# Kernel optimization log

Hardware: AMD Instinct MI355X
Metric: run time of the kernel (lower is better)

## Reference

```python
import jax, jax.numpy as jnp
import numpy as np

N, E = 50000, 800000
F_IN, HID, CLS, K = 128, 128, 40, 4


def setup_inputs() -> dict:
    key = jax.random.key(0)
    ks = jax.random.split(key, 6)
    x = jax.random.normal(ks[0], (N, F_IN), jnp.float32)
    edge_src = jax.random.randint(ks[1], (E,), 0, N, jnp.int32)
    edge_dst = jax.random.randint(ks[2], (E,), 0, N, jnp.int32)
    glorot = lambda k, sh, fan: jax.random.normal(k, sh, jnp.float32) * np.float32(1.0 / np.sqrt(fan))
    W0 = glorot(ks[3], (K, F_IN, HID), F_IN)
    W1 = glorot(ks[4], (K, HID, HID), HID)
    W2 = glorot(ks[5], (K, HID, CLS), HID)
    b0 = jnp.zeros((HID,), jnp.float32)
    b1 = jnp.zeros((HID,), jnp.float32)
    b2 = jnp.zeros((CLS,), jnp.float32)
    return dict(x=x, edge_src=edge_src, edge_dst=edge_dst,
                W0=W0, b0=b0, W1=W1, b1=b1, W2=W2, b2=b2)


def _cheb_edge_norm(edge_src, edge_dst, n):
    # PyG ChebConv 'sym' norm with lambda_max=2: scaled Laplacian
    # L_hat = 2L/lambda_max - I = -D^{-1/2} A D^{-1/2}  (diagonal is exactly 0)
    ones = jnp.ones(edge_src.shape[0], jnp.float32)
    deg = jax.ops.segment_sum(ones, edge_src, num_segments=n)
    dinv = jnp.where(deg > 0, jax.lax.rsqrt(jnp.maximum(deg, 1.0)), 0.0)
    return -dinv[edge_src] * dinv[edge_dst]  # [E]


def _cheb_conv(x, edge_src, edge_dst, w_norm, W, b, n):
    # Chebyshev recurrence: Tx0 = x, Tx1 = L_hat x, Tx_k = 2 L_hat Tx_{k-1} - Tx_{k-2}
    def lhat(t):  # SpMM: out[dst] += w * t[src]
        return jax.ops.segment_sum(t[edge_src] * w_norm[:, None], edge_dst, num_segments=n)

    Tx0 = x
    out = Tx0 @ W[0]
    Tx1 = lhat(Tx0)
    out = out + Tx1 @ W[1]
    for k in range(2, W.shape[0]):
        Tx2 = 2.0 * lhat(Tx1) - Tx0
        out = out + Tx2 @ W[k]
        Tx0, Tx1 = Tx1, Tx2
    return out + b


def reference(x, edge_src, edge_dst, W0, b0, W1, b1, W2, b2):
    n = x.shape[0]
    w_norm = _cheb_edge_norm(edge_src, edge_dst, n)
    h = x
    x1 = h
    for W, b in ((W0, b0), (W1, b1), (W2, b2)):
        x1 = _cheb_conv(h, edge_src, edge_dst, w_norm, W, b, n)
        h = jax.nn.relu(x1)  # dropout(p=0.6) is identity in eval mode
    # original returns log_softmax of the LAST conv's pre-activation x1
    return jax.nn.log_softmax(x1, axis=1)
```

## Files before the change

### kernel.cpp

```cpp
#include <hip/hip_runtime.h>
#include <math.h>

#define NN 50000
#define NE 800000
#define FDIM 128
#define CLS 40
#define AW 512
#define ZW 256
#define RSLOT 64

typedef __attribute__((ext_vector_type(8))) short short8v;
typedef __attribute__((ext_vector_type(8))) unsigned short ushort8v;
typedef __attribute__((ext_vector_type(4))) float f32x4;

__device__ inline float b2f(unsigned short u) {
    union { unsigned int i; float f; } v; v.i = ((unsigned)u) << 16; return v.f;
}
__device__ inline unsigned short f2b(float f) {
    unsigned int x = __float_as_uint(f);
    unsigned int r = (x + 0x7fffu + ((x >> 16) & 1u)) >> 16;
    return (unsigned short)r;
}


__global__ void zero_k(int* degi, int* fill) {
    int i = blockIdx.x * blockDim.x + threadIdx.x;
    if (i < NN) { degi[i] = 0; fill[i] = 0; }
}

#define NB_ES   782
#define NB_CVT  3125
#define NB_WH   256
#define NB_WZ   128

__global__ __launch_bounds__(256) void prep_k(
        const int4* __restrict__ esrc4, const int4* __restrict__ edst4,
        int* degi, int* fill, int* __restrict__ ews,
        const float* __restrict__ x, unsigned short* __restrict__ Ab,
        const float* __restrict__ W0, const float* __restrict__ W1,
        const float* __restrict__ W2,
        unsigned short* __restrict__ Wt0, unsigned short* __restrict__ Wt1,
        unsigned short* __restrict__ Wz) {
    int b = blockIdx.x;
    int tid = threadIdx.x;
    if (b < NB_ES) {
        int e = b * 256 + tid;
        if (e < NE / 4) {
            int4 s = esrc4[e], d = edst4[e];
            atomicAdd(&degi[s.x], 1); atomicAdd(&degi[s.y], 1);
            atomicAdd(&degi[s.z], 1); atomicAdd(&degi[s.w], 1);
            int c0 = atomicAdd(&fill[d.x], 1);
            int c1 = atomicAdd(&fill[d.y], 1);
            int c2 = atomicAdd(&fill[d.z], 1);
            int c3 = atomicAdd(&fill[d.w], 1);
            if (c0 < RSLOT) ews[d.x * RSLOT + c0] = s.x;
            if (c1 < RSLOT) ews[d.y * RSLOT + c1] = s.y;
            if (c2 < RSLOT) ews[d.z * RSLOT + c2] = s.z;
            if (c3 < RSLOT) ews[d.w * RSLOT + c3] = s.w;
        }
    } else if (b < NB_ES + NB_CVT) {
        int i = (b - NB_ES) * 256 + tid;
        int row = i >> 4, cg = i & 15;
        const float4* xp = (const float4*)(x + (size_t)row * FDIM + cg * 8);
        float4 v0 = xp[0], v1 = xp[1];
        ushort8v r;
        r[0] = f2b(v0.x); r[1] = f2b(v0.y); r[2] = f2b(v0.z); r[3] = f2b(v0.w);
        r[4] = f2b(v1.x); r[5] = f2b(v1.y); r[6] = f2b(v1.z); r[7] = f2b(v1.w);
        *(ushort8v*)(Ab + (size_t)row * AW + cg * 8) = r;
    } else if (b < NB_ES + NB_CVT + 2 * NB_WH) {
        int wi = b - NB_ES - NB_CVT;
        const float* W = (wi < NB_WH) ? W0 : W1;
        unsigned short* Wfm = (wi < NB_WH) ? Wt0 : Wt1;
        int i = (wi % NB_WH) * 256 + tid;
        int j = i & 7, l = (i >> 3) & 63, kcl = (i >> 9) & 3, nt = (i >> 11) & 7, c = i >> 14;
        int r = kcl * 32 + (l >> 4) * 8 + j;
        int col = nt * 16 + (l & 15);
        Wfm[i] = f2b(W[((size_t)c * 128 + r) * 128 + col]);
    } else {
        int i = (b - NB_ES - NB_CVT - 2 * NB_WH) * 256 + tid;
        int j = i & 7, l = (i >> 3) & 63, kcl = (i >> 9) & 3, nt = (i >> 11) & 7, half = (i >> 14) & 1;
        int k = kcl * 32 + (l >> 4) * 8 + j;
        int col = half * 128 + nt * 16 + (l & 15);
        int kcheb = col >> 6, cc = col & 63;
        float v = (cc < CLS) ? W2[((size_t)kcheb * 128 + k) * CLS + cc] : 0.0f;
        Wz[i] = f2b(v);
    }
}

__global__ void dinv_k(const int* __restrict__ degi, float* __restrict__ dinv) {
    int i = blockIdx.x * blockDim.x + threadIdx.x;
    if (i < NN) {
        int d = degi[i];
        dinv[i] = (d > 0) ? rsqrtf((float)d) : 0.0f;
    }
}


template <bool CHEB>
__global__ __launch_bounds__(256) void spmm_k(const unsigned short* __restrict__ inp,
                                              const unsigned short* __restrict__ prevp,
                                              unsigned short* __restrict__ outp,
                                              const int* __restrict__ fill,
                                              const int* __restrict__ ews,
                                              const float* __restrict__ dinv) {
    int row = blockIdx.x * 4 + (threadIdx.x >> 6);
    int lane = threadIdx.x & 63;
    int slot = lane >> 4, ln = lane & 15;
    int n = fill[row];
    if (n > RSLOT) n = RSLOT;
    int e0 = row * RSLOT, e1 = e0 + n;
    float dvr = dinv[row];
    float acc[8] = {0.f, 0.f, 0.f, 0.f, 0.f, 0.f, 0.f, 0.f};
    int e = e0;
    for (; e + 8 <= e1; e += 8) {
        int2 s01 = *(const int2*)&ews[e + slot * 2];
        ushort8v t0 = *(const ushort8v*)(inp + (size_t)s01.x * AW + ln * 8);
        ushort8v t1 = *(const ushort8v*)(inp + (size_t)s01.y * AW + ln * 8);
        float w0 = -dinv[s01.x] * dvr, w1 = -dinv[s01.y] * dvr;
        #pragma unroll
        for (int j = 0; j < 8; j++)
            acc[j] += w0 * b2f(t0[j]) + w1 * b2f(t1[j]);
    }
    for (; e < e1; e += 4) {
        int ee = e + slot;
        int s = (ee < e1) ? ews[ee] : 0;
        float w = (ee < e1) ? (-dinv[s] * dvr) : 0.0f;
        ushort8v t = *(const ushort8v*)(inp + (size_t)s * AW + ln * 8);
        #pragma unroll
        for (int j = 0; j < 8; j++) acc[j] += w * b2f(t[j]);
    }
    #pragma unroll
    for (int j = 0; j < 8; j++) {
        acc[j] += __shfl_xor(acc[j], 16);
        acc[j] += __shfl_xor(acc[j], 32);
    }
    if (slot == 0) {
        ushort8v r;
        if (CHEB) {
            ushort8v p = *(const ushort8v*)(prevp + (size_t)row * AW + ln * 8);
            #pragma unroll
            for (int j = 0; j < 8; j++) r[j] = f2b(2.f * acc[j] - b2f(p[j]));
        } else {
            #pragma unroll
            for (int j = 0; j < 8; j++) r[j] = f2b(acc[j]);
        }
        *(ushort8v*)(outp + (size_t)row * AW + ln * 8) = r;
    }
}


template <int MODE>
__global__ __launch_bounds__(256) void spmm64_k(const unsigned short* __restrict__ gsrc,
                                                const unsigned short* __restrict__ zadd,
                                                const unsigned short* __restrict__ bsub,
                                                unsigned short* __restrict__ wout,
                                                float* __restrict__ fout,
                                                const int* __restrict__ fill,
                                                const int* __restrict__ ews,
                                                const float* __restrict__ dinv) {
    constexpr int GS = (MODE == 0) ? ZW : 64;
    constexpr float SC = (MODE == 2) ? 1.0f : 2.0f;
    int row = blockIdx.x * 4 + (threadIdx.x >> 6);
    int lane = threadIdx.x & 63;
    int slot = lane >> 3, ln = lane & 7;
    int n = fill[row];
    if (n > RSLOT) n = RSLOT;
    int e0 = row * RSLOT, e1 = e0 + n;
    float dvr = dinv[row];
    float acc[8] = {0.f, 0.f, 0.f, 0.f, 0.f, 0.f, 0.f, 0.f};
    int e = e0;
    for (; e + 16 <= e1; e += 16) {
        int2 s01 = *(const int2*)&ews[e + slot * 2];
        ushort8v t0 = *(const ushort8v*)(gsrc + (size_t)s01.x * GS + ln * 8);
        ushort8v t1 = *(const ushort8v*)(gsrc + (size_t)s01.y * GS + ln * 8);
        float w0 = -dinv[s01.x] * dvr, w1 = -dinv[s01.y] * dvr;
        #pragma unroll
        for (int j = 0; j < 8; j++)
            acc[j] += w0 * b2f(t0[j]) + w1 * b2f(t1[j]);
    }
    for (; e < e1; e += 8) {
        int ee = e + slot;
        int s = (ee < e1) ? ews[ee] : 0;
        float w = (ee < e1) ? (-dinv[s] * dvr) : 0.0f;
        ushort8v t = *(const ushort8v*)(gsrc + (size_t)s * GS + ln * 8);
        #pragma unroll
        for (int j = 0; j < 8; j++) acc[j] += w * b2f(t[j]);
    }
    #pragma unroll
    for (int j = 0; j < 8; j++) {
        acc[j] += __shfl_xor(acc[j], 8);
        acc[j] += __shfl_xor(acc[j], 16);
        acc[j] += __shfl_xor(acc[j], 32);
    }
    if (slot != 0) return;
    ushort8v zv = *(const ushort8v*)(zadd + (size_t)row * ZW + ln * 8);
    float v[8];
    if (MODE == 0) {
        #pragma unroll
        for (int j = 0; j < 8; j++) v[j] = b2f(zv[j]) + SC * acc[j];
    } else {
        constexpr int BS = (MODE == 1) ? ZW : 64;
        ushort8v bv = *(const ushort8v*)(bsub + (size_t)row * BS + ln * 8);
        #pragma unroll
        for (int j = 0; j < 8; j++) v[j] = b2f(zv[j]) + SC * acc[j] - b2f(bv[j]);
    }
    if (MODE < 2) {
        ushort8v r;
        #pragma unroll
        for (int j = 0; j < 8; j++) r[j] = f2b(v[j]);
        *(ushort8v*)(wout + (size_t)row * 64 + ln * 8) = r;
    } else {
        float m = -INFINITY;
        #pragma unroll
        for (int j = 0; j < 8; j++) if (ln * 8 + j < CLS) m = fmaxf(m, v[j]);
        #pragma unroll
        for (int off = 4; off >= 1; off >>= 1) m = fmaxf(m, __shfl_xor(m, off));
        float s = 0.f;
        #pragma unroll
        for (int j = 0; j < 8; j++) if (ln * 8 + j < CLS) s += __expf(v[j] - m);
        #pragma unroll
        for (int off = 4; off >= 1; off >>= 1) s += __shfl_xor(s, off);
        float ls = logf(s) + m;
        #pragma unroll
        for (int j = 0; j < 8; j++) {
            int col = ln * 8 + j;
            if (col < CLS) fout[(size_t)row * CLS + col] = v[j] - ls;
        }
    }
}


__global__ __launch_bounds__(256) void gemm_hid_k(const unsigned short* __restrict__ A,
                                                  const unsigned short* __restrict__ Wfm,
                                                  const float* __restrict__ bias,
                                                  unsigned short* __restrict__ Hout) {
    __shared__ unsigned short Blds[16384];
    int tid = threadIdx.x;
    int w = tid >> 6, lane = tid & 63, ln = lane & 15, gp = lane >> 4;
    int rowbase = blockIdx.x * 64 + w * 16;
    int rowc = rowbase + ln;
    if (rowc >= NN) rowc = NN - 1;
    const unsigned short* Arow = A + (size_t)rowc * AW + gp * 8;

    f32x4 acc[8];
    #pragma unroll
    for (int i = 0; i < 8; i++) acc[i] = (f32x4){0.f, 0.f, 0.f, 0.f};

    short8v acur[4], anxt[4];
    #pragma unroll
    for (int kcl = 0; kcl < 4; kcl++) acur[kcl] = *(const short8v*)(Arow + kcl * 32);
    {
        const ushort8v* g = (const ushort8v*)Wfm;
        ushort8v* s = (ushort8v*)Blds;
        #pragma unroll
        for (int i = 0; i < 8; i++) s[tid + i * 256] = g[tid + i * 256];
    }
    __syncthreads();

    for (int c = 0; c < 4; c++) {
        if (c < 3) {
            #pragma unroll
            for (int kcl = 0; kcl < 4; kcl++)
                anxt[kcl] = *(const short8v*)(Arow + (c + 1) * 128 + kcl * 32);
        }
        #pragma unroll
        for (int kcl = 0; kcl < 4; kcl++) {
            #pragma unroll
            for (int nt = 0; nt < 8; nt++) {
                short8v b = *(const short8v*)&Blds[((nt * 4 + kcl) * 64 + lane) * 8];
                acc[nt] = __builtin_amdgcn_mfma_f32_16x16x32_bf16(acur[kcl], b, acc[nt], 0, 0, 0);
            }
        }
        if (c < 3) {
            __syncthreads();
            const ushort8v* g = (const ushort8v*)(Wfm + (c + 1) * 16384);
            ushort8v* s = (ushort8v*)Blds;
            #pragma unroll
            for (int i = 0; i < 8; i++) s[tid + i * 256] = g[tid + i * 256];
            __syncthreads();
            #pragma unroll
            for (int kcl = 0; kcl < 4; kcl++) acur[kcl] = anxt[kcl];
        }
    }

    if (rowbase < NN) {
        #pragma unroll
        for (int nt = 0; nt < 8; nt++) {
            int col = nt * 16 + ln;
            float bv = bias[col];
            #pragma unroll
            for (int j = 0; j < 4; j++) {
                int r = rowbase + gp * 4 + j;
                Hout[(size_t)r * AW + col] = f2b(fmaxf(acc[nt][j] + bv, 0.0f));
            }
        }
    }
}


__global__ __launch_bounds__(256) void gemm_z_k(const unsigned short* __restrict__ A,
                                                const unsigned short* __restrict__ Wz,
                                                const float* __restrict__ b2,
                                                unsigned short* __restrict__ Z) {
    __shared__ unsigned short Blds[16384];
    int tid = threadIdx.x;
    int w = tid >> 6, lane = tid & 63, ln = lane & 15, gp = lane >> 4;
    int rowbase = blockIdx.x * 64 + w * 16;
    int rowc = rowbase + ln;
    if (rowc >= NN) rowc = NN - 1;
    const unsigned short* Arow = A + (size_t)rowc * AW + gp * 8;

    short8v af[4];
    #pragma unroll
    for (int kcl = 0; kcl < 4; kcl++) af[kcl] = *(const short8v*)(Arow + kcl * 32);

    for (int half = 0; half < 2; half++) {
        if (half) __syncthreads();
        {
            const ushort8v* g = (const ushort8v*)(Wz + half * 16384);
            ushort8v* s = (ushort8v*)Blds;
            #pragma unroll
            for (int i = 0; i < 8; i++) s[tid + i * 256] = g[tid + i * 256];
        }
        __syncthreads();
        f32x4 acc[8];
        #pragma unroll
        for (int i = 0; i < 8; i++) acc[i] = (f32x4){0.f, 0.f, 0.f, 0.f};
        #pragma unroll
        for (int kcl = 0; kcl < 4; kcl++) {
            #pragma unroll
            for (int nt = 0; nt < 8; nt++) {
                short8v b = *(const short8v*)&Blds[((nt * 4 + kcl) * 64 + lane) * 8];
                acc[nt] = __builtin_amdgcn_mfma_f32_16x16x32_bf16(af[kcl], b, acc[nt], 0, 0, 0);
            }
        }
        if (rowbase < NN) {
            #pragma unroll
            for (int nt = 0; nt < 8; nt++) {
                int col = half * 128 + nt * 16 + ln;
                float bv = (col < CLS) ? b2[col] : 0.0f;
                #pragma unroll
                for (int j = 0; j < 4; j++) {
                    int r = rowbase + gp * 4 + j;
                    Z[(size_t)r * ZW + col] = f2b(acc[nt][j] + bv);
                }
            }
        }
    }
}


extern "C" void kernel_launch(void* const* d_in, const int* in_sizes, int n_in,
                              void* d_out, int out_size, void* d_ws, size_t ws_size,
                              hipStream_t stream) {
    const float* x    = (const float*)d_in[0];
    const int*   esrc = (const int*)d_in[1];
    const int*   edst = (const int*)d_in[2];
    const float* W0   = (const float*)d_in[3];
    const float* b0   = (const float*)d_in[4];
    const float* W1   = (const float*)d_in[5];
    const float* b1   = (const float*)d_in[6];
    const float* W2   = (const float*)d_in[7];
    const float* b2   = (const float*)d_in[8];
    float* out = (float*)d_out;

    char* p = (char*)d_ws;
    auto alloc = [&](size_t bytes) -> void* {
        void* r = (void*)p;
        p += (bytes + 255) & ~(size_t)255;
        return r;
    };
    unsigned short* Abuf = (unsigned short*)alloc((size_t)NN * AW * 2);
    unsigned short* Zbuf = (unsigned short*)alloc((size_t)NN * ZW * 2);
    unsigned short* B1b  = (unsigned short*)alloc((size_t)NN * 64 * 2);
    unsigned short* B2b  = (unsigned short*)alloc((size_t)NN * 64 * 2);
    int*   ews  = (int*)alloc((size_t)NN * RSLOT * 4);
    unsigned short* Wt0  = (unsigned short*)alloc((size_t)128 * AW * 2);
    unsigned short* Wt1  = (unsigned short*)alloc((size_t)128 * AW * 2);
    unsigned short* Wz   = (unsigned short*)alloc((size_t)32768 * 2);
    int*   degi = (int*)alloc(NN * 4);
    int*   fill = (int*)alloc(NN * 4);
    float* dinv = (float*)alloc(NN * 4);

    const int TB = 256;
    int gN = (NN + TB - 1) / TB;

    zero_k<<<gN, TB, 0, stream>>>(degi, fill);
    prep_k<<<NB_ES + NB_CVT + 2 * NB_WH + NB_WZ, TB, 0, stream>>>(
        (const int4*)esrc, (const int4*)edst, degi, fill, ews,
        x, Abuf, W0, W1, W2, Wt0, Wt1, Wz);
    dinv_k<<<gN, TB, 0, stream>>>(degi, dinv);

    int gSpmm = (NN + 3) / 4;
    int gGemm = (NN + 63) / 64;

    unsigned short* s0 = Abuf + 0 * 128;
    unsigned short* s1 = Abuf + 1 * 128;
    unsigned short* s2 = Abuf + 2 * 128;
    unsigned short* s3 = Abuf + 3 * 128;

    for (int l = 0; l < 2; l++) {
        spmm_k<false><<<gSpmm, TB, 0, stream>>>(s0, nullptr, s1, fill, ews, dinv);
        spmm_k<true><<<gSpmm, TB, 0, stream>>>(s1, s0, s2, fill, ews, dinv);
        spmm_k<true><<<gSpmm, TB, 0, stream>>>(s2, s1, s3, fill, ews, dinv);
        const unsigned short* Wt = (l == 0) ? Wt0 : Wt1;
        const float* bl = (l == 0) ? b0 : b1;
        gemm_hid_k<<<gGemm, TB, 0, stream>>>(Abuf, Wt, bl, Abuf);
    }

    gemm_z_k<<<gGemm, TB, 0, stream>>>(Abuf, Wz, b2, Zbuf);
    spmm64_k<0><<<gSpmm, TB, 0, stream>>>(Zbuf + 192, Zbuf + 128, nullptr,
                                          B2b, nullptr, fill, ews, dinv);
    spmm64_k<1><<<gSpmm, TB, 0, stream>>>(B2b, Zbuf + 64, Zbuf + 192,
                                          B1b, nullptr, fill, ews, dinv);
    spmm64_k<2><<<gSpmm, TB, 0, stream>>>(B1b, Zbuf, B2b,
                                          nullptr, out, fill, ews, dinv);
}
```

Baseline: 427.5 us.

## Pad edge slots with sentinel node to remove SpMM tail loops and widen gathers

Prefills the per-row edge slot array with a sentinel index NN whose dinv is zero, and adds one padding row to each feature buffer. The SpMM kernels can then run a single loop over the degree rounded up, with no remainder loop, loading four edge indices per lane and issuing four independent row gathers per iteration. This should raise memory-level parallelism and remove divergent tail handling. In exchange, zero_k now writes the full 12.8 MB slot array, and sentinel edges still issue gathers. The sentinel row's feature values are never explicitly zeroed, so the result relies on the zero weight.

```diff
diff --git a/kernel.cpp b/kernel.cpp
--- a/kernel.cpp
+++ b/kernel.cpp
@@ -23,9 +23,23 @@
 }
 
 
-__global__ void zero_k(int* degi, int* fill) {
-    int i = blockIdx.x * blockDim.x + threadIdx.x;
-    if (i < NN) { degi[i] = 0; fill[i] = 0; }
+#define NB_Z0 196
+#define NB_Z1 782
+
+__global__ __launch_bounds__(256) void zero_k(int* degi, int* fill, int4* ews4) {
+    int b = blockIdx.x;
+    if (b < NB_Z0) {
+        int i = b * 256 + threadIdx.x;
+        if (i < NN) { degi[i] = 0; fill[i] = 0; }
+    } else {
+        int base = (b - NB_Z0) * 1024;
+        int4 v = make_int4(NN, NN, NN, NN);
+        #pragma unroll
+        for (int j = 0; j < 4; j++) {
+            int idx = base + j * 256 + threadIdx.x;
+            if (idx < NN * RSLOT / 4) ews4[idx] = v;
+        }
+    }
 }
 
 #define NB_ES   782
@@ -92,6 +106,8 @@
     if (i < NN) {
         int d = degi[i];
         dinv[i] = (d > 0) ? rsqrtf((float)d) : 0.0f;
+    } else if (i == NN) {
+        dinv[i] = 0.0f;
     }
 }
 
@@ -108,26 +124,21 @@
     int slot = lane >> 4, ln = lane & 15;
     int n = fill[row];
     if (n > RSLOT) n = RSLOT;
-    int e0 = row * RSLOT, e1 = e0 + n;
+    int nr = (n + 15) & ~15;
+    int e0 = row * RSLOT;
     float dvr = dinv[row];
     float acc[8] = {0.f, 0.f, 0.f, 0.f, 0.f, 0.f, 0.f, 0.f};
-    int e = e0;
-    for (; e + 8 <= e1; e += 8) {
-        int2 s01 = *(const int2*)&ews[e + slot * 2];
-        ushort8v t0 = *(const ushort8v*)(inp + (size_t)s01.x * AW + ln * 8);
-        ushort8v t1 = *(const ushort8v*)(inp + (size_t)s01.y * AW + ln * 8);
-        float w0 = -dinv[s01.x] * dvr, w1 = -dinv[s01.y] * dvr;
+    for (int e = e0; e < e0 + nr; e += 16) {
+        int4 s4 = *(const int4*)&ews[e + slot * 4];
+        ushort8v t0 = *(const ushort8v*)(inp + (size_t)s4.x * AW + ln * 8);
+        ushort8v t1 = *(const ushort8v*)(inp + (size_t)s4.y * AW + ln * 8);
+        ushort8v t2 = *(const ushort8v*)(inp + (size_t)s4.z * AW + ln * 8);
+        ushort8v t3 = *(const ushort8v*)(inp + (size_t)s4.w * AW + ln * 8);
+        float w0 = -dinv[s4.x] * dvr, w1 = -dinv[s4.y] * dvr;
+        float w2 = -dinv[s4.z] * dvr, w3 = -dinv[s4.w] * dvr;
         #pragma unroll
         for (int j = 0; j < 8; j++)
-            acc[j] += w0 * b2f(t0[j]) + w1 * b2f(t1[j]);
-    }
-    for (; e < e1; e += 4) {
-        int ee = e + slot;
-        int s = (ee < e1) ? ews[ee] : 0;
-        float w = (ee < e1) ? (-dinv[s] * dvr) : 0.0f;
-        ushort8v t = *(const ushort8v*)(inp + (size_t)s * AW + ln * 8);
-        #pragma unroll
-        for (int j = 0; j < 8; j++) acc[j] += w * b2f(t[j]);
+            acc[j] += w0 * b2f(t0[j]) + w1 * b2f(t1[j]) + w2 * b2f(t2[j]) + w3 * b2f(t3[j]);
     }
     #pragma unroll
     for (int j = 0; j < 8; j++) {
@@ -165,26 +176,21 @@
     int slot = lane >> 3, ln = lane & 7;
     int n = fill[row];
     if (n > RSLOT) n = RSLOT;
-    int e0 = row * RSLOT, e1 = e0 + n;
+    int nr = (n + 31) & ~31;
+    int e0 = row * RSLOT;
     float dvr = dinv[row];
     float acc[8] = {0.f, 0.f, 0.f, 0.f, 0.f, 0.f, 0.f, 0.f};
-    int e = e0;
-    for (; e + 16 <= e1; e += 16) {
-        int2 s01 = *(const int2*)&ews[e + slot * 2];
-        ushort8v t0 = *(const ushort8v*)(gsrc + (size_t)s01.x * GS + ln * 8);
-        ushort8v t1 = *(const ushort8v*)(gsrc + (size_t)s01.y * GS + ln * 8);
-        float w0 = -dinv[s01.x] * dvr, w1 = -dinv[s01.y] * dvr;
+    for (int e = e0; e < e0 + nr; e += 32) {
+        int4 s4 = *(const int4*)&ews[e + slot * 4];
+        ushort8v t0 = *(const ushort8v*)(gsrc + (size_t)s4.x * GS + ln * 8);
+        ushort8v t1 = *(const ushort8v*)(gsrc + (size_t)s4.y * GS + ln * 8);
+        ushort8v t2 = *(const ushort8v*)(gsrc + (size_t)s4.z * GS + ln * 8);
+        ushort8v t3 = *(const ushort8v*)(gsrc + (size_t)s4.w * GS + ln * 8);
+        float w0 = -dinv[s4.x] * dvr, w1 = -dinv[s4.y] * dvr;
+        float w2 = -dinv[s4.z] * dvr, w3 = -dinv[s4.w] * dvr;
         #pragma unroll
         for (int j = 0; j < 8; j++)
-            acc[j] += w0 * b2f(t0[j]) + w1 * b2f(t1[j]);
-    }
-    for (; e < e1; e += 8) {
-        int ee = e + slot;
-        int s = (ee < e1) ? ews[ee] : 0;
-        float w = (ee < e1) ? (-dinv[s] * dvr) : 0.0f;
-        ushort8v t = *(const ushort8v*)(gsrc + (size_t)s * GS + ln * 8);
-        #pragma unroll
-        for (int j = 0; j < 8; j++) acc[j] += w * b2f(t[j]);
+            acc[j] += w0 * b2f(t0[j]) + w1 * b2f(t1[j]) + w2 * b2f(t2[j]) + w3 * b2f(t3[j]);
     }
     #pragma unroll
     for (int j = 0; j < 8; j++) {
@@ -370,26 +376,26 @@
         p += (bytes + 255) & ~(size_t)255;
         return r;
     };
-    unsigned short* Abuf = (unsigned short*)alloc((size_t)NN * AW * 2);
-    unsigned short* Zbuf = (unsigned short*)alloc((size_t)NN * ZW * 2);
-    unsigned short* B1b  = (unsigned short*)alloc((size_t)NN * 64 * 2);
-    unsigned short* B2b  = (unsigned short*)alloc((size_t)NN * 64 * 2);
+    unsigned short* Abuf = (unsigned short*)alloc((size_t)(NN + 1) * AW * 2);
+    unsigned short* Zbuf = (unsigned short*)alloc((size_t)(NN + 1) * ZW * 2);
+    unsigned short* B1b  = (unsigned short*)alloc((size_t)(NN + 1) * 64 * 2);
+    unsigned short* B2b  = (unsigned short*)alloc((size_t)(NN + 1) * 64 * 2);
     int*   ews  = (int*)alloc((size_t)NN * RSLOT * 4);
     unsigned short* Wt0  = (unsigned short*)alloc((size_t)128 * AW * 2);
     unsigned short* Wt1  = (unsigned short*)alloc((size_t)128 * AW * 2);
     unsigned short* Wz   = (unsigned short*)alloc((size_t)32768 * 2);
     int*   degi = (int*)alloc(NN * 4);
     int*   fill = (int*)alloc(NN * 4);
-    float* dinv = (float*)alloc(NN * 4);
+    float* dinv = (float*)alloc((NN + 1) * 4);
 
     const int TB = 256;
-    int gN = (NN + TB - 1) / TB;
-
-    zero_k<<<gN, TB, 0, stream>>>(degi, fill);
+    int gN1 = (NN + 1 + TB - 1) / TB;
+
+    zero_k<<<NB_Z0 + NB_Z1, TB, 0, stream>>>(degi, fill, (int4*)ews);
     prep_k<<<NB_ES + NB_CVT + 2 * NB_WH + NB_WZ, TB, 0, stream>>>(
         (const int4*)esrc, (const int4*)edst, degi, fill, ews,
         x, Abuf, W0, W1, W2, Wt0, Wt1, Wz);
-    dinv_k<<<gN, TB, 0, stream>>>(degi, dinv);
+    dinv_k<<<gN1, TB, 0, stream>>>(degi, dinv);
 
     int gSpmm = (NN + 3) / 4;
     int gGemm = (NN + 63) / 64;
```

Result: faster. 396.2 us (-7.3%).
